# Kernel optimization log

Measured on AMD Instinct MI355X. Metric: run time of the kernel, lower is better.

Reference implementation:

```python
import jax, jax.numpy as jnp
import numpy as np

B, C, H = 256, 5, 13
N_AGENTS = 8192
N_EDGES = 262144
ACT = 21


def setup_inputs() -> dict:
    key = jax.random.key(0)
    ks = jax.random.split(key, 20)
    inp = {
        "x": jax.random.normal(ks[0], (B, C, H, H), jnp.float32),
        "x_msg": jax.random.normal(ks[1], (N_AGENTS,), jnp.float32),
        "edge_index": jax.random.randint(ks[2], (N_EDGES, 2), 0, N_AGENTS, jnp.int64 if jax.config.jax_enable_x64 else jnp.int32),
        "action": jax.random.randint(ks[3], (B,), 0, ACT, jnp.int32),
        # params (orthogonal init approximated by scaled normal; math identical)
        "conv1_w": jax.random.normal(ks[4], (32, 5, 3, 3), jnp.float32) * 0.1,
        "conv1_b": jnp.zeros((32,), jnp.float32),
        "conv2_w": jax.random.normal(ks[5], (64, 32, 3, 3), jnp.float32) * 0.05,
        "conv2_b": jnp.zeros((64,), jnp.float32),
        "fc_w": jax.random.normal(ks[6], (512, 1024), jnp.float32) * 0.03,
        "fc_b": jnp.zeros((512,), jnp.float32),
        "fc_mu_w": jax.random.normal(ks[7], (ACT, 512), jnp.float32) * 0.01,
        "fc_mu_b": jnp.zeros((ACT,), jnp.float32),
        "msg_w": jax.random.normal(ks[8], (N_AGENTS, 512), jnp.float32) * 0.01,
        "msg_b": jnp.zeros((N_AGENTS,), jnp.float32),
        "gcn1_w": jax.random.normal(ks[9], (2, 16), jnp.float32) * 0.5,
        "gcn1_b": jnp.zeros((16,), jnp.float32),
        "gcn2_w": jax.random.normal(ks[10], (16, N_AGENTS), jnp.float32) * 0.1,
        "gcn2_b": jnp.zeros((N_AGENTS,), jnp.float32),
    }
    return inp


def _gcn_norm(edge_index, n):
    # add self-loops; edge_index is (E,2) [src, dst]
    loops = jnp.arange(n, dtype=edge_index.dtype)
    src = jnp.concatenate([edge_index[:, 0], loops])
    dst = jnp.concatenate([edge_index[:, 1], loops])
    deg = jax.ops.segment_sum(jnp.ones_like(src, jnp.float32), dst, num_segments=n)
    dinv = jnp.where(deg > 0, jax.lax.rsqrt(deg), 0.0)
    norm = dinv[src] * dinv[dst]  # [E+n]
    return src, dst, norm


def _gcn_conv(h, src, dst, norm, W, b, n):
    hw = h @ W  # [n, out]
    out = jax.ops.segment_sum(norm[:, None] * hw[src], dst, num_segments=n)
    return out + b


def reference(x, x_msg, edge_index, action, conv1_w, conv1_b, conv2_w, conv2_b,
              fc_w, fc_b, fc_mu_w, fc_mu_b, msg_w, msg_b,
              gcn1_w, gcn1_b, gcn2_w, gcn2_b):
    dn = ("NCHW", "OIHW", "NCHW")
    h = jax.lax.conv_general_dilated(x, conv1_w, (2, 2), "VALID", dimension_numbers=dn)
    h = jax.nn.relu(h + conv1_b[None, :, None, None])  # [B,32,6,6]
    h = jax.lax.conv_general_dilated(h, conv2_w, (1, 1), "VALID", dimension_numbers=dn)
    h = jax.nn.relu(h + conv2_b[None, :, None, None])  # [B,64,4,4]
    h = h.reshape(h.shape[0], -1)  # [B,1024], torch NCHW flatten order
    hidden = jax.nn.relu(h @ fc_w.T + fc_b)  # [B,512]

    logits = hidden @ fc_mu_w.T + fc_mu_b            # [B,21]
    actor_encoding = hidden @ msg_w.T + msg_b        # [B,N]

    # Categorical log_prob / entropy for the given action
    logp = jax.nn.log_softmax(logits, axis=-1)
    log_prob = jnp.take_along_axis(logp, action[:, None], axis=1)[:, 0]
    entropy = -jnp.sum(jnp.exp(logp) * logp, axis=-1)

    # GNN message branch (eval mode: dropout is identity)
    feats = jnp.stack([x_msg, actor_encoding[0]], axis=0).T  # [N,2]
    n = feats.shape[0]
    src, dst, norm = _gcn_norm(edge_index, n)
    g = jax.nn.relu(_gcn_conv(feats, src, dst, norm, gcn1_w, gcn1_b, n))  # [N,16]
    g = _gcn_conv(g, src, dst, norm, gcn2_w, gcn2_b, n)                    # [N,N]
    msg_out = jax.nn.log_softmax(g, axis=1).mean(axis=1)                   # [N]

    return (action, msg_out, log_prob, entropy)
```

## Files before the change

kernel.cpp:

```cpp
#include <hip/hip_runtime.h>
#include <hip/hip_bf16.h>

#define NB 256
#define NACT 21
#define NA 8192
#define NE 262144
#define CSR_CAP 128
#define LOG2E 1.44269504f

#if __has_builtin(__builtin_amdgcn_exp2f)
#define EXP2F(x) __builtin_amdgcn_exp2f(x)
#else
#define EXP2F(x) exp2f(x)
#endif

typedef __attribute__((ext_vector_type(8))) short short8;
typedef __attribute__((ext_vector_type(4))) float float4v;

__device__ inline float wsum64(float v) {
#pragma unroll
  for (int m = 32; m > 0; m >>= 1) v += __shfl_xor(v, m, 64);
  return v;
}

__device__ inline unsigned short f2bf(float f) {
  union { __hip_bfloat16 h; unsigned short u; } cv;
  cv.h = __float2bfloat16(f);
  return cv.u;
}

__global__ __launch_bounds__(512, 2) void k_ic(
    const float* __restrict__ x, const float* __restrict__ c1w, const float* __restrict__ c1b_,
    const float* __restrict__ c2w, unsigned short* c1b, unsigned short* w2abf, int* cnt) {
  __shared__ float sm[3437];
  int t = threadIdx.x, b = blockIdx.x;
  if (b >= 272) {
    int i = (b - 272) * 512 + t;
    w2abf[i] = f2bf(c2w[i]);
    return;
  }
  if (b >= 256) {
    cnt[(b - 256) * 512 + t] = 0;
    return;
  }
  float* xs = sm;
  float* w1s = sm + 845;
  float* c1s = sm + 2285;
  for (int i = t; i < 845; i += 512) xs[i] = x[b * 845 + i];
  for (int i = t; i < 1440; i += 512) w1s[i] = c1w[i];
  __syncthreads();
  for (int idx = t; idx < 1152; idx += 512) {
    int oc = idx / 36, p = idx - oc * 36;
    int oy = p / 6, ox = p - oy * 6;
    float acc = c1b_[oc];
    const float* wp = &w1s[oc * 45];
#pragma unroll
    for (int ic = 0; ic < 5; ic++)
#pragma unroll
      for (int ky = 0; ky < 3; ky++)
#pragma unroll
        for (int kx = 0; kx < 3; kx++)
          acc += xs[ic * 169 + (oy * 2 + ky) * 13 + ox * 2 + kx] * wp[ic * 9 + ky * 3 + kx];
    c1s[idx] = fmaxf(acc, 0.0f);
  }
  __syncthreads();
  for (int i = t; i < 4608; i += 512) {
    int p = i / 288, k = i - p * 288;
    int ic = k / 9, r = k - ic * 9;
    int ky = r / 3, kx = r - ky * 3;
    int oy = p >> 2, ox = p & 3;
    c1b[b * 4608 + i] = f2bf(c1s[ic * 36 + (oy + ky) * 6 + ox + kx]);
  }
}

__global__ __launch_bounds__(512, 2) void k_pc(
    const int* __restrict__ edges, const float* __restrict__ fcw,
    const float* __restrict__ g2w, const float* __restrict__ g2b,
    unsigned short* fcwbf, unsigned short* w2t, float* wpart, int* cnt, int* csr,
    const unsigned short* __restrict__ c1b, const unsigned short* __restrict__ w2abf,
    const float* __restrict__ c2b, unsigned short* h1024bf) {
  __shared__ float sm[288];
  int t = threadIdx.x;
  int wave = t >> 6, lane = t & 63;
  if (blockIdx.x < 512) {
    float (*red)[17] = (float(*)[17])sm;
    float* b2s = sm + 272;
    int blk = blockIdx.x;
    {
      int e = blk * 512 + t;
      int s = edges[2 * e], d = edges[2 * e + 1];
      int slot = atomicAdd(&cnt[d], 1);
      if (slot < CSR_CAP) csr[d * CSR_CAP + slot] = s;
    }
    {
      int base = (blk * 512 + t) * 2;
      float2 v = *(const float2*)&fcw[base];
      fcwbf[base + 0] = f2bf(v.x);
      fcwbf[base + 1] = f2bf(v.y);
    }
    {
      if (t < 256) {
        int jj = t >> 4, k = t & 15;
        int j = blk * 16 + jj;
        float w = g2w[k * 8192 + j];
        w2t[j * 16 + k] = f2bf(w);
        red[jj][k] = w;
      }
      if (t < 16) b2s[t] = g2b[blk * 16 + t];
      __syncthreads();
      if (t < 16) {
        float s = 0.0f;
#pragma unroll
        for (int q = 0; q < 16; q++) s += red[q][t];
        wpart[blk * 17 + t] = s;
      } else if (t == 16) {
        float s = 0.0f;
#pragma unroll
        for (int q = 0; q < 16; q++) s += b2s[q];
        wpart[blk * 17 + 16] = s;
      }
    }
  } else {
    int nb = blockIdx.x - 512;
    int nbase = nb * 256 + wave * 32;
    int m = lane & 15, quad = lane >> 4;
    float4v z = {0.0f, 0.0f, 0.0f, 0.0f};
    float4v acc00 = z, acc01 = z, acc02 = z, acc03 = z;
    float4v acc10 = z, acc11 = z, acc12 = z, acc13 = z;
#pragma unroll
    for (int ks = 0; ks < 9; ks++) {
      int ko = ks * 32 + quad * 8;
      short8 a0 = *(const short8*)&w2abf[(0 * 16 + m) * 288 + ko];
      short8 a1 = *(const short8*)&w2abf[(1 * 16 + m) * 288 + ko];
      short8 a2 = *(const short8*)&w2abf[(2 * 16 + m) * 288 + ko];
      short8 a3 = *(const short8*)&w2abf[(3 * 16 + m) * 288 + ko];
      short8 b0 = *(const short8*)&c1b[(nbase + m) * 288 + ko];
      short8 b1 = *(const short8*)&c1b[(nbase + 16 + m) * 288 + ko];
      acc00 = __builtin_amdgcn_mfma_f32_16x16x32_bf16(a0, b0, acc00, 0, 0, 0);
      acc01 = __builtin_amdgcn_mfma_f32_16x16x32_bf16(a1, b0, acc01, 0, 0, 0);
      acc02 = __builtin_amdgcn_mfma_f32_16x16x32_bf16(a2, b0, acc02, 0, 0, 0);
      acc03 = __builtin_amdgcn_mfma_f32_16x16x32_bf16(a3, b0, acc03, 0, 0, 0);
      acc10 = __builtin_amdgcn_mfma_f32_16x16x32_bf16(a0, b1, acc10, 0, 0, 0);
      acc11 = __builtin_amdgcn_mfma_f32_16x16x32_bf16(a1, b1, acc11, 0, 0, 0);
      acc12 = __builtin_amdgcn_mfma_f32_16x16x32_bf16(a2, b1, acc12, 0, 0, 0);
      acc13 = __builtin_amdgcn_mfma_f32_16x16x32_bf16(a3, b1, acc13, 0, 0, 0);
    }
    float4v accs[2][4] = {{acc00, acc01, acc02, acc03}, {acc10, acc11, acc12, acc13}};
#pragma unroll
    for (int nt = 0; nt < 2; nt++) {
#pragma unroll
      for (int mt = 0; mt < 4; mt++) {
#pragma unroll
        for (int r = 0; r < 4; r++) {
          int oc = mt * 16 + quad * 4 + r;
          int n = nbase + nt * 16 + m;
          int img = n >> 4, pos = n & 15;
          h1024bf[img * 1024 + oc * 16 + pos] =
              f2bf(fmaxf(accs[nt][mt][r] + c2b[oc], 0.0f));
        }
      }
    }
  }
}

__global__ __launch_bounds__(256, 4) void k_fc(
    const int* __restrict__ cnt, const float* __restrict__ x_msg,
    const unsigned short* __restrict__ h1024bf, const unsigned short* __restrict__ fcwbf,
    const float* __restrict__ fcb, const float* __restrict__ wpart,
    float* hidden, float* dinv, float* xs2, float* wsf) {
  __shared__ float red[4][256];
  int t = threadIdx.x, blk = blockIdx.x;
  if (blk == 512) {
    float* part = &red[0][0];
    if (t < 272) {
      int q = t / 17, c = t - q * 17;
      float s = 0.0f;
      for (int r = q; r < 512; r += 16) s += wpart[r * 17 + c];
      part[t] = s;
    }
    __syncthreads();
    if (t < 17) {
      float s = 0.0f;
#pragma unroll
      for (int q = 0; q < 16; q++) s += part[q * 17 + t];
      wsf[t] = s;
    }
    return;
  }
  int wave = t >> 6, lane = t & 63;
  if (blk < 32) {
    int i = blk * 256 + t;
    float d = rsqrtf((float)cnt[i] + 1.0f);
    dinv[i] = d;
    xs2[i] = d * x_msg[i];
  }
  int tr = blk >> 5, tc = blk & 31;
  int m = lane & 15, quad = lane >> 4;
  const unsigned short* ap = &h1024bf[(tr * 16 + m) * 1024 + wave * 256 + quad * 8];
  const unsigned short* bp = &fcwbf[(tc * 16 + m) * 1024 + wave * 256 + quad * 8];
  float4v acc = {0.0f, 0.0f, 0.0f, 0.0f};
#pragma unroll
  for (int i = 0; i < 8; i++) {
    short8 a = *(const short8*)(ap + i * 32);
    short8 b = *(const short8*)(bp + i * 32);
    acc = __builtin_amdgcn_mfma_f32_16x16x32_bf16(a, b, acc, 0, 0, 0);
  }
#pragma unroll
  for (int r = 0; r < 4; r++) red[wave][(quad * 4 + r) * 16 + m] = acc[r];
  __syncthreads();
  {
    float s = red[0][t] + red[1][t] + red[2][t] + red[3][t];
    int gr = tr * 16 + (t >> 4);
    int gc = tc * 16 + (t & 15);
    hidden[gr * 512 + gc] = fmaxf(s + fcb[gc], 0.0f);
  }
}

__global__ __launch_bounds__(512, 2) void k_he(
    const float* __restrict__ hidden, const float* __restrict__ muw,
    const float* __restrict__ mub, const float* __restrict__ msgw,
    const float* __restrict__ msgb, const float* __restrict__ dinv,
    const int* __restrict__ action, float* es2, float* out) {
  __shared__ float muT[10752];
  __shared__ float hrows[2048];
  int t = threadIdx.x, blk = blockIdx.x;
  int wave = t >> 6, lane = t & 63;
  if (blk < 64) {
    int b0 = blk * 4;
    for (int i = t; i < 10752; i += 512) {
      int a = i >> 9, k = i & 511;
      muT[k * 21 + a] = muw[i];
    }
    for (int i = t; i < 2048; i += 512) hrows[i] = hidden[b0 * 512 + i];
    __syncthreads();
    if (wave < 4) {
      int b = b0 + wave;
      float logit = -1e30f;
      if (lane < NACT) {
        float acc = mub[lane];
        const float* hr = &hrows[wave * 512];
        for (int k = 0; k < 512; k++) acc += hr[k] * muT[k * 21 + lane];
        logit = acc;
      }
      float m = logit;
#pragma unroll
      for (int s = 32; s > 0; s >>= 1) m = fmaxf(m, __shfl_xor(m, s, 64));
      float e = (lane < NACT) ? __expf(logit - m) : 0.0f;
      float se = wsum64(e);
      float swl = wsum64(e * logit);
      float lse = m + __logf(se);
      int act = action[b];
      if (lane == 0) {
        out[b] = (float)act;
        out[8704 + b] = lse - swl / se;
      }
      if (lane == act) out[8448 + b] = logit - lse;
    }
  } else {
    int wg = (blk - 64) * 8 + wave;
    for (int j = wg; j < NA; j += 3584) {
      const float* wp = &msgw[j * 512 + lane * 8];
      float4 w0 = *(const float4*)(wp);
      float4 w1 = *(const float4*)(wp + 4);
      float4 h0 = *(const float4*)&hidden[lane * 8];
      float4 h1 = *(const float4*)&hidden[lane * 8 + 4];
      float s = w0.x * h0.x + w0.y * h0.y + w0.z * h0.z + w0.w * h0.w +
                w1.x * h1.x + w1.y * h1.y + w1.z * h1.z + w1.w * h1.w;
      s = wsum64(s);
      if (lane == 0) es2[j] = dinv[j] * (s + msgb[j]);
    }
  }
}

__global__ __launch_bounds__(512, 4) void k_g1(
    const int* __restrict__ cnt, const int* __restrict__ csr,
    const float* __restrict__ dinv, const float* __restrict__ xs2,
    const float* __restrict__ es2, const float* __restrict__ g1w,
    const float* __restrict__ g1b, float* gbuf2) {
  int t = threadIdx.x, blk = blockIdx.x;
  int wave = t >> 6, lane = t & 63;
  int wg = blk * 8 + wave;
#pragma unroll
  for (int rr = 0; rr < 2; rr++) {
    int i = wg * 2 + rr;
    int ci = min(cnt[i], CSR_CAP);
    float di = dinv[i];
    float a0 = 0.0f, a1 = 0.0f;
    for (int e = lane; e < ci; e += 64) {
      int s = csr[i * CSR_CAP + e];
      a0 += xs2[s];
      a1 += es2[s];
    }
    float f0 = (wsum64(a0) + xs2[i]) * di;
    float f1 = (wsum64(a1) + es2[i]) * di;
    if (lane < 16) {
      float gv = fmaxf(f0 * g1w[lane] + f1 * g1w[16 + lane] + g1b[lane], 0.0f);
      gbuf2[i * 16 + lane] = di * gv;
    }
  }
}

__global__ __launch_bounds__(512, 2) void k_msg(
    const int* __restrict__ cnt, const int* __restrict__ csr,
    const float* __restrict__ dinv, const float* __restrict__ gbuf2,
    const float* __restrict__ wsf, const unsigned short* __restrict__ w2t,
    const float* __restrict__ g2b, float* out) {
  __shared__ __align__(16) unsigned short vbf[256];
  __shared__ float vf[256];
  __shared__ float pl[2048];
  __shared__ float sl[128];
  __shared__ float wsfs[17];
  int t = threadIdx.x, blk = blockIdx.x;
  int wave = t >> 6, lane = t & 63;
  int rowbase = blk * 16;
  if (t < 17) wsfs[t] = wsf[t];
  {
    int eq = lane >> 4, c = lane & 15;
#pragma unroll
    for (int rr = 0; rr < 2; rr++) {
      int il = wave * 2 + rr;
      int i = rowbase + il;
      int ci = min(cnt[i], CSR_CAP);
      float di = dinv[i];
      float acc = (eq == 0) ? gbuf2[i * 16 + c] : 0.0f;
      for (int e = eq; e < ci; e += 4) {
        int s = csr[i * CSR_CAP + e];
        acc += gbuf2[s * 16 + c];
      }
      acc *= di;
      acc += __shfl_xor(acc, 16, 64);
      acc += __shfl_xor(acc, 32, 64);
      if (eq == 0) {
        vf[il * 16 + c] = acc;
        vbf[il * 16 + c] = f2bf(acc * LOG2E);
      }
    }
  }
  __syncthreads();
  float myMean = 0.0f;
  if (t < 16) {
    float dot = 0.0f;
#pragma unroll
    for (int c = 0; c < 16; c++) dot += vf[t * 16 + c] * wsfs[c];
    myMean = (dot + wsfs[16]) * (1.0f / 8192.0f);
  }
  {
    int quad = lane >> 4, n = lane & 15;
    int k8 = quad * 8;
    short8 za = {0, 0, 0, 0, 0, 0, 0, 0};
    short8 a1 = za;
    if (quad < 2) a1 = *(const short8*)&vbf[n * 16 + k8];
    float sacc[4];
#pragma unroll
    for (int q = 0; q < 4; q++) sacc[q] = 0.0f;
    int colb = wave * 1024 + n;
    for (int tp = 0; tp < 64; tp += 2) {
      int col1 = colb + tp * 16;
      int col2 = col1 + 16;
      short8 b1 = za, b2 = za;
      if (quad < 2) {
        b1 = *(const short8*)&w2t[col1 * 16 + k8];
        b2 = *(const short8*)&w2t[col2 * 16 + k8];
      }
      float bb1 = g2b[col1] * LOG2E, bb2 = g2b[col2] * LOG2E;
      float4v c1 = {bb1, bb1, bb1, bb1};
      float4v c2 = {bb2, bb2, bb2, bb2};
      float4v s11 = __builtin_amdgcn_mfma_f32_16x16x32_bf16(a1, b1, c1, 0, 0, 0);
      float4v s12 = __builtin_amdgcn_mfma_f32_16x16x32_bf16(a1, b2, c2, 0, 0, 0);
#pragma unroll
      for (int r = 0; r < 4; r++) sacc[r] += EXP2F(s11[r]) + EXP2F(s12[r]);
    }
#pragma unroll
    for (int q = 0; q < 4; q++) {
      int rl = quad * 4 + q;
      pl[rl * 128 + wave * 16 + n] = sacc[q];
    }
  }
  __syncthreads();
  if (t < 128) {
    int r = t >> 3, seg = t & 7;
    int base = r * 128 + seg * 16;
    float ll = 0.0f;
#pragma unroll
    for (int i = 0; i < 16; i++) ll += pl[base + i];
    sl[r * 8 + seg] = ll;
  }
  __syncthreads();
  if (t < 16) {
    float ll = 0.0f;
#pragma unroll
    for (int i = 0; i < 8; i++) ll += sl[t * 8 + i];
    out[256 + rowbase + t] = myMean - __logf(ll);
  }
}

extern "C" void kernel_launch(void* const* d_in, const int* in_sizes, int n_in,
                              void* d_out, int out_size, void* d_ws, size_t ws_size,
                              hipStream_t stream) {
  const float* x     = (const float*)d_in[0];
  const float* x_msg = (const float*)d_in[1];
  const int*   edges = (const int*)d_in[2];
  const int*   action= (const int*)d_in[3];
  const float* c1w   = (const float*)d_in[4];
  const float* c1bb  = (const float*)d_in[5];
  const float* c2w   = (const float*)d_in[6];
  const float* c2b   = (const float*)d_in[7];
  const float* fcw   = (const float*)d_in[8];
  const float* fcb   = (const float*)d_in[9];
  const float* muw   = (const float*)d_in[10];
  const float* mub   = (const float*)d_in[11];
  const float* msgw  = (const float*)d_in[12];
  const float* msgb  = (const float*)d_in[13];
  const float* g1w   = (const float*)d_in[14];
  const float* g1b   = (const float*)d_in[15];
  const float* g2w   = (const float*)d_in[16];
  const float* g2b   = (const float*)d_in[17];
  float* out = (float*)d_out;

  float* ws     = (float*)d_ws;
  unsigned short* h1024bf = (unsigned short*)ws;
  unsigned short* fcwbf   = (unsigned short*)(ws + 131072);
  float* hidden = ws + 393216;
  float* es2    = ws + 524288;
  float* dinv   = ws + 532480;
  float* xs2    = ws + 540672;
  float* gbuf2  = ws + 548864;
  float* wpart  = ws + 679936;
  unsigned short* w2t = (unsigned short*)(ws + 688640);
  int*   cnt    = (int*)(ws + 754176);
  int*   csr    = (int*)(ws + 762368);
  float* wsf    = ws + 1810944;
  unsigned short* c1b   = (unsigned short*)(ws + 1810964);
  unsigned short* w2abf = (unsigned short*)(ws + 2400788);

  k_ic <<<308, 512, 0, stream>>>(x, c1w, c1bb, c2w, c1b, w2abf, cnt);
  k_pc <<<528, 512, 0, stream>>>(edges, fcw, g2w, g2b, fcwbf, w2t, wpart, cnt, csr,
                                 c1b, w2abf, c2b, h1024bf);
  k_fc <<<513, 256, 0, stream>>>(cnt, x_msg, h1024bf, fcwbf, fcb, wpart, hidden, dinv, xs2, wsf);
  k_he <<<512, 512, 0, stream>>>(hidden, muw, mub, msgw, msgb, dinv, action, es2, out);
  k_g1 <<<512, 512, 0, stream>>>(cnt, csr, dinv, xs2, es2, g1w, g1b, gbuf2);
  k_msg<<<512, 512, 0, stream>>>(cnt, csr, dinv, gbuf2, wsf, w2t, g2b, out);
}
```

Measured before the change: 174.2 us.

## Fuse FC layer with actor head and message encoding into one kernel

Merges the FC GEMM kernel and the head/encoding kernel into a single launch. Each block recomputes its 16-row hidden tile in LDS as bf16, so the hidden matrix never goes through global memory. The actor logits move to MFMA, and the message-encoding blocks recompute hidden row 0 redundantly. This drops one launch and the global round-trip but adds redundant FC work across 80 blocks, uses a small grid of 97 blocks, and lowers hidden and mu-weight precision to bf16.

New measurement: 220.6 us. 26.7% more time.

```diff
diff --git a/kernel.cpp b/kernel.cpp
--- a/kernel.cpp
+++ b/kernel.cpp
@@ -27,6 +27,12 @@
   union { __hip_bfloat16 h; unsigned short u; } cv;
   cv.h = __float2bfloat16(f);
   return cv.u;
+}
+
+__device__ inline float bf2f(unsigned short u) {
+  union { unsigned int u; float f; } cv;
+  cv.u = ((unsigned int)u) << 16;
+  return cv.f;
 }
 
 __global__ __launch_bounds__(512, 2) void k_ic(
@@ -163,111 +169,116 @@
   }
 }
 
-__global__ __launch_bounds__(256, 4) void k_fc(
+__global__ __launch_bounds__(512, 2) void k_fhe(
     const int* __restrict__ cnt, const float* __restrict__ x_msg,
     const unsigned short* __restrict__ h1024bf, const unsigned short* __restrict__ fcwbf,
-    const float* __restrict__ fcb, const float* __restrict__ wpart,
-    float* hidden, float* dinv, float* xs2, float* wsf) {
-  __shared__ float red[4][256];
-  int t = threadIdx.x, blk = blockIdx.x;
-  if (blk == 512) {
-    float* part = &red[0][0];
+    const float* __restrict__ fcb, const float* __restrict__ muw, const float* __restrict__ mub,
+    const float* __restrict__ msgw, const float* __restrict__ msgb,
+    const int* __restrict__ action, const float* __restrict__ wpart,
+    float* es2, float* dinv, float* xs2, float* wsf, float* out) {
+  __shared__ __align__(16) unsigned short hidbf[8192];
+  __shared__ float smf[512];
+  int t = threadIdx.x, b = blockIdx.x;
+  int wave = t >> 6, lane = t & 63;
+  if (b >= 96) {
     if (t < 272) {
       int q = t / 17, c = t - q * 17;
       float s = 0.0f;
       for (int r = q; r < 512; r += 16) s += wpart[r * 17 + c];
-      part[t] = s;
+      smf[t] = s;
     }
     __syncthreads();
     if (t < 17) {
       float s = 0.0f;
 #pragma unroll
-      for (int q = 0; q < 16; q++) s += part[q * 17 + t];
+      for (int q = 0; q < 16; q++) s += smf[q * 17 + t];
       wsf[t] = s;
     }
     return;
   }
-  int wave = t >> 6, lane = t & 63;
-  if (blk < 32) {
-    int i = blk * 256 + t;
+  if (b >= 80) {
+    int i = (b - 80) * 512 + t;
     float d = rsqrtf((float)cnt[i] + 1.0f);
     dinv[i] = d;
     xs2[i] = d * x_msg[i];
-  }
-  int tr = blk >> 5, tc = blk & 31;
+    return;
+  }
+  int r0 = (b < 16) ? b * 16 : 0;
   int m = lane & 15, quad = lane >> 4;
-  const unsigned short* ap = &h1024bf[(tr * 16 + m) * 1024 + wave * 256 + quad * 8];
-  const unsigned short* bp = &fcwbf[(tc * 16 + m) * 1024 + wave * 256 + quad * 8];
-  float4v acc = {0.0f, 0.0f, 0.0f, 0.0f};
-#pragma unroll
-  for (int i = 0; i < 8; i++) {
-    short8 a = *(const short8*)(ap + i * 32);
-    short8 b = *(const short8*)(bp + i * 32);
-    acc = __builtin_amdgcn_mfma_f32_16x16x32_bf16(a, b, acc, 0, 0, 0);
-  }
-#pragma unroll
-  for (int r = 0; r < 4; r++) red[wave][(quad * 4 + r) * 16 + m] = acc[r];
-  __syncthreads();
   {
-    float s = red[0][t] + red[1][t] + red[2][t] + red[3][t];
-    int gr = tr * 16 + (t >> 4);
-    int gc = tc * 16 + (t & 15);
-    hidden[gr * 512 + gc] = fmaxf(s + fcb[gc], 0.0f);
-  }
-}
-
-__global__ __launch_bounds__(512, 2) void k_he(
-    const float* __restrict__ hidden, const float* __restrict__ muw,
-    const float* __restrict__ mub, const float* __restrict__ msgw,
-    const float* __restrict__ msgb, const float* __restrict__ dinv,
-    const int* __restrict__ action, float* es2, float* out) {
-  __shared__ float muT[10752];
-  __shared__ float hrows[2048];
-  int t = threadIdx.x, blk = blockIdx.x;
-  int wave = t >> 6, lane = t & 63;
-  if (blk < 64) {
-    int b0 = blk * 4;
-    for (int i = t; i < 10752; i += 512) {
-      int a = i >> 9, k = i & 511;
-      muT[k * 21 + a] = muw[i];
-    }
-    for (int i = t; i < 2048; i += 512) hrows[i] = hidden[b0 * 512 + i];
+    const unsigned short* ap = &h1024bf[(r0 + m) * 1024 + quad * 8];
+#pragma unroll
+    for (int tc = 0; tc < 4; tc++) {
+      int col0 = wave * 64 + tc * 16;
+      const unsigned short* bp = &fcwbf[(col0 + m) * 1024 + quad * 8];
+      float4v acc = {0.0f, 0.0f, 0.0f, 0.0f};
+#pragma unroll
+      for (int ks = 0; ks < 32; ks++) {
+        short8 av = *(const short8*)(ap + ks * 32);
+        short8 bv = *(const short8*)(bp + ks * 32);
+        acc = __builtin_amdgcn_mfma_f32_16x16x32_bf16(av, bv, acc, 0, 0, 0);
+      }
+#pragma unroll
+      for (int r = 0; r < 4; r++) {
+        int i = quad * 4 + r;
+        hidbf[i * 512 + col0 + m] = f2bf(fmaxf(acc[r] + fcb[col0 + m], 0.0f));
+      }
+    }
+  }
+  __syncthreads();
+  if (b < 16) {
+    if (wave < 2) {
+      int col0 = wave * 16;
+      int act_i = col0 + m;
+      float bias = (act_i < NACT) ? mub[act_i] : 0.0f;
+      float4v acc = {bias, bias, bias, bias};
+#pragma unroll
+      for (int ks = 0; ks < 16; ks++) {
+        short8 av = *(const short8*)&hidbf[m * 512 + ks * 32 + quad * 8];
+        short8 bv = {0, 0, 0, 0, 0, 0, 0, 0};
+        if (act_i < NACT) {
+          const float* wp = &muw[act_i * 512 + ks * 32 + quad * 8];
+#pragma unroll
+          for (int q2 = 0; q2 < 8; q2++) bv[q2] = (short)f2bf(wp[q2]);
+        }
+        acc = __builtin_amdgcn_mfma_f32_16x16x32_bf16(av, bv, acc, 0, 0, 0);
+      }
+#pragma unroll
+      for (int r = 0; r < 4; r++) smf[(quad * 4 + r) * 32 + col0 + m] = acc[r];
+    }
     __syncthreads();
-    if (wave < 4) {
-      int b = b0 + wave;
-      float logit = -1e30f;
-      if (lane < NACT) {
-        float acc = mub[lane];
-        const float* hr = &hrows[wave * 512];
-        for (int k = 0; k < 512; k++) acc += hr[k] * muT[k * 21 + lane];
-        logit = acc;
-      }
-      float m = logit;
-#pragma unroll
-      for (int s = 32; s > 0; s >>= 1) m = fmaxf(m, __shfl_xor(m, s, 64));
-      float e = (lane < NACT) ? __expf(logit - m) : 0.0f;
+#pragma unroll
+    for (int rr = 0; rr < 2; rr++) {
+      int rloc = wave * 2 + rr;
+      int bb = r0 + rloc;
+      float logit = (lane < NACT) ? smf[rloc * 32 + lane] : -1e30f;
+      float mx = logit;
+#pragma unroll
+      for (int s = 32; s > 0; s >>= 1) mx = fmaxf(mx, __shfl_xor(mx, s, 64));
+      float e = (lane < NACT) ? __expf(logit - mx) : 0.0f;
       float se = wsum64(e);
       float swl = wsum64(e * logit);
-      float lse = m + __logf(se);
-      int act = action[b];
+      float lse = mx + __logf(se);
+      int act = action[bb];
       if (lane == 0) {
-        out[b] = (float)act;
-        out[8704 + b] = lse - swl / se;
-      }
-      if (lane == act) out[8448 + b] = logit - lse;
+        out[bb] = (float)act;
+        out[8704 + bb] = lse - swl / se;
+      }
+      if (lane == act) out[8448 + bb] = logit - lse;
     }
   } else {
-    int wg = (blk - 64) * 8 + wave;
-    for (int j = wg; j < NA; j += 3584) {
+    float h0[8];
+#pragma unroll
+    for (int q2 = 0; q2 < 8; q2++) h0[q2] = bf2f(hidbf[lane * 8 + q2]);
+    int jbase = (b - 16) * 128 + wave * 16;
+    for (int j = jbase; j < jbase + 16; j++) {
       const float* wp = &msgw[j * 512 + lane * 8];
       float4 w0 = *(const float4*)(wp);
       float4 w1 = *(const float4*)(wp + 4);
-      float4 h0 = *(const float4*)&hidden[lane * 8];
-      float4 h1 = *(const float4*)&hidden[lane * 8 + 4];
-      float s = w0.x * h0.x + w0.y * h0.y + w0.z * h0.z + w0.w * h0.w +
-                w1.x * h1.x + w1.y * h1.y + w1.z * h1.z + w1.w * h1.w;
+      float s = w0.x * h0[0] + w0.y * h0[1] + w0.z * h0[2] + w0.w * h0[3] +
+                w1.x * h0[4] + w1.y * h0[5] + w1.z * h0[6] + w1.w * h0[7];
       s = wsum64(s);
-      if (lane == 0) es2[j] = dinv[j] * (s + msgb[j]);
+      if (lane == 0) es2[j] = rsqrtf((float)cnt[j] + 1.0f) * (s + msgb[j]);
     }
   }
 }
@@ -420,7 +431,6 @@
   float* ws     = (float*)d_ws;
   unsigned short* h1024bf = (unsigned short*)ws;
   unsigned short* fcwbf   = (unsigned short*)(ws + 131072);
-  float* hidden = ws + 393216;
   float* es2    = ws + 524288;
   float* dinv   = ws + 532480;
   float* xs2    = ws + 540672;
@@ -436,8 +446,8 @@
   k_ic <<<308, 512, 0, stream>>>(x, c1w, c1bb, c2w, c1b, w2abf, cnt);
   k_pc <<<528, 512, 0, stream>>>(edges, fcw, g2w, g2b, fcwbf, w2t, wpart, cnt, csr,
                                  c1b, w2abf, c2b, h1024bf);
-  k_fc <<<513, 256, 0, stream>>>(cnt, x_msg, h1024bf, fcwbf, fcb, wpart, hidden, dinv, xs2, wsf);
-  k_he <<<512, 512, 0, stream>>>(hidden, muw, mub, msgw, msgb, dinv, action, es2, out);
+  k_fhe<<<97, 512, 0, stream>>>(cnt, x_msg, h1024bf, fcwbf, fcb, muw, mub, msgw, msgb,
+                                action, wpart, es2, dinv, xs2, wsf, out);
   k_g1 <<<512, 512, 0, stream>>>(cnt, csr, dinv, xs2, es2, g1w, g1b, gbuf2);
   k_msg<<<512, 512, 0, stream>>>(cnt, csr, dinv, gbuf2, wsf, w2t, g2b, out);
 }
```

## Fuse conv2 into FC GEMM via LDS and merge prep kernels

Applied to the files above, without the earlier changes.

Moves the weight-conversion and wpart work into the first kernel, and fuses the conv2 MFMA with the FC GEMM. Each FC block now recomputes its 16-image conv2 tile into shared memory, so the h1024 global round trip is gone. Edge CSR building moves to the fused kernel, and the dinv/xs2 computation moves to k_he, which recomputes rsqrt inline. This removes one kernel launch and a global intermediate. In exchange, the conv2 tile is computed redundantly 32 times, once per column block.

Result: no change. 175.9 us (+1.0%).

```diff
diff --git a/kernel.cpp b/kernel.cpp
--- a/kernel.cpp
+++ b/kernel.cpp
@@ -29,69 +29,18 @@
   return cv.u;
 }
 
-__global__ __launch_bounds__(512, 2) void k_ic(
+__global__ __launch_bounds__(512, 2) void k_ip(
     const float* __restrict__ x, const float* __restrict__ c1w, const float* __restrict__ c1b_,
-    const float* __restrict__ c2w, unsigned short* c1b, unsigned short* w2abf, int* cnt) {
+    const float* __restrict__ c2w, const float* __restrict__ fcw,
+    const float* __restrict__ g2w, const float* __restrict__ g2b,
+    unsigned short* c1b, unsigned short* w2abf, int* cnt,
+    unsigned short* fcwbf, unsigned short* w2t, float* wpart) {
   __shared__ float sm[3437];
   int t = threadIdx.x, b = blockIdx.x;
-  if (b >= 272) {
-    int i = (b - 272) * 512 + t;
-    w2abf[i] = f2bf(c2w[i]);
-    return;
-  }
-  if (b >= 256) {
-    cnt[(b - 256) * 512 + t] = 0;
-    return;
-  }
-  float* xs = sm;
-  float* w1s = sm + 845;
-  float* c1s = sm + 2285;
-  for (int i = t; i < 845; i += 512) xs[i] = x[b * 845 + i];
-  for (int i = t; i < 1440; i += 512) w1s[i] = c1w[i];
-  __syncthreads();
-  for (int idx = t; idx < 1152; idx += 512) {
-    int oc = idx / 36, p = idx - oc * 36;
-    int oy = p / 6, ox = p - oy * 6;
-    float acc = c1b_[oc];
-    const float* wp = &w1s[oc * 45];
-#pragma unroll
-    for (int ic = 0; ic < 5; ic++)
-#pragma unroll
-      for (int ky = 0; ky < 3; ky++)
-#pragma unroll
-        for (int kx = 0; kx < 3; kx++)
-          acc += xs[ic * 169 + (oy * 2 + ky) * 13 + ox * 2 + kx] * wp[ic * 9 + ky * 3 + kx];
-    c1s[idx] = fmaxf(acc, 0.0f);
-  }
-  __syncthreads();
-  for (int i = t; i < 4608; i += 512) {
-    int p = i / 288, k = i - p * 288;
-    int ic = k / 9, r = k - ic * 9;
-    int ky = r / 3, kx = r - ky * 3;
-    int oy = p >> 2, ox = p & 3;
-    c1b[b * 4608 + i] = f2bf(c1s[ic * 36 + (oy + ky) * 6 + ox + kx]);
-  }
-}
-
-__global__ __launch_bounds__(512, 2) void k_pc(
-    const int* __restrict__ edges, const float* __restrict__ fcw,
-    const float* __restrict__ g2w, const float* __restrict__ g2b,
-    unsigned short* fcwbf, unsigned short* w2t, float* wpart, int* cnt, int* csr,
-    const unsigned short* __restrict__ c1b, const unsigned short* __restrict__ w2abf,
-    const float* __restrict__ c2b, unsigned short* h1024bf) {
-  __shared__ float sm[288];
-  int t = threadIdx.x;
-  int wave = t >> 6, lane = t & 63;
-  if (blockIdx.x < 512) {
+  if (b >= 308) {
     float (*red)[17] = (float(*)[17])sm;
     float* b2s = sm + 272;
-    int blk = blockIdx.x;
-    {
-      int e = blk * 512 + t;
-      int s = edges[2 * e], d = edges[2 * e + 1];
-      int slot = atomicAdd(&cnt[d], 1);
-      if (slot < CSR_CAP) csr[d * CSR_CAP + slot] = s;
-    }
+    int blk = b - 308;
     {
       int base = (blk * 512 + t) * 2;
       float2 v = *(const float2*)&fcw[base];
@@ -120,10 +69,85 @@
         wpart[blk * 17 + 16] = s;
       }
     }
-  } else {
-    int nb = blockIdx.x - 512;
-    int nbase = nb * 256 + wave * 32;
-    int m = lane & 15, quad = lane >> 4;
+    return;
+  }
+  if (b >= 272) {
+    int i = (b - 272) * 512 + t;
+    w2abf[i] = f2bf(c2w[i]);
+    return;
+  }
+  if (b >= 256) {
+    cnt[(b - 256) * 512 + t] = 0;
+    return;
+  }
+  float* xs = sm;
+  float* w1s = sm + 845;
+  float* c1s = sm + 2285;
+  for (int i = t; i < 845; i += 512) xs[i] = x[b * 845 + i];
+  for (int i = t; i < 1440; i += 512) w1s[i] = c1w[i];
+  __syncthreads();
+  for (int idx = t; idx < 1152; idx += 512) {
+    int oc = idx / 36, p = idx - oc * 36;
+    int oy = p / 6, ox = p - oy * 6;
+    float acc = c1b_[oc];
+    const float* wp = &w1s[oc * 45];
+#pragma unroll
+    for (int ic = 0; ic < 5; ic++)
+#pragma unroll
+      for (int ky = 0; ky < 3; ky++)
+#pragma unroll
+        for (int kx = 0; kx < 3; kx++)
+          acc += xs[ic * 169 + (oy * 2 + ky) * 13 + ox * 2 + kx] * wp[ic * 9 + ky * 3 + kx];
+    c1s[idx] = fmaxf(acc, 0.0f);
+  }
+  __syncthreads();
+  for (int i = t; i < 4608; i += 512) {
+    int p = i / 288, k = i - p * 288;
+    int ic = k / 9, r = k - ic * 9;
+    int ky = r / 3, kx = r - ky * 3;
+    int oy = p >> 2, ox = p & 3;
+    c1b[b * 4608 + i] = f2bf(c1s[ic * 36 + (oy + ky) * 6 + ox + kx]);
+  }
+}
+
+__global__ __launch_bounds__(512, 2) void k_cf(
+    const int* __restrict__ edges, int* cnt, int* csr,
+    const unsigned short* __restrict__ c1b, const unsigned short* __restrict__ w2abf,
+    const float* __restrict__ c2b, const unsigned short* __restrict__ fcwbf,
+    const float* __restrict__ fcb, const float* __restrict__ wpart,
+    float* hidden, float* wsf) {
+  __shared__ __align__(16) unsigned short hs[16384];
+  __shared__ float red[2048];
+  int t = threadIdx.x, blk = blockIdx.x;
+  int wave = t >> 6, lane = t & 63;
+  int m = lane & 15, quad = lane >> 4;
+  if (blk >= 1024) {
+    if (t < 272) {
+      int q = t / 17, c = t - q * 17;
+      float s = 0.0f;
+      for (int r = q; r < 512; r += 16) s += wpart[r * 17 + c];
+      red[t] = s;
+    }
+    __syncthreads();
+    if (t < 17) {
+      float s = 0.0f;
+#pragma unroll
+      for (int q = 0; q < 16; q++) s += red[q * 17 + t];
+      wsf[t] = s;
+    }
+    return;
+  }
+  if (blk >= 512) {
+    int e = (blk - 512) * 512 + t;
+    int s = edges[2 * e], d = edges[2 * e + 1];
+    int slot = atomicAdd(&cnt[d], 1);
+    if (slot < CSR_CAP) csr[d * CSR_CAP + slot] = s;
+    return;
+  }
+  int tr = blk >> 5, tc = blk & 31;
+  {
+    int nlb = wave * 32;
+    int nbase = tr * 256 + nlb;
     float4v z = {0.0f, 0.0f, 0.0f, 0.0f};
     float4v acc00 = z, acc01 = z, acc02 = z, acc03 = z;
     float4v acc10 = z, acc11 = z, acc12 = z, acc13 = z;
@@ -153,78 +177,55 @@
 #pragma unroll
         for (int r = 0; r < 4; r++) {
           int oc = mt * 16 + quad * 4 + r;
-          int n = nbase + nt * 16 + m;
-          int img = n >> 4, pos = n & 15;
-          h1024bf[img * 1024 + oc * 16 + pos] =
+          int nl = nlb + nt * 16 + m;
+          hs[(nl >> 4) * 1024 + oc * 16 + (nl & 15)] =
               f2bf(fmaxf(accs[nt][mt][r] + c2b[oc], 0.0f));
         }
       }
     }
   }
-}
-
-__global__ __launch_bounds__(256, 4) void k_fc(
-    const int* __restrict__ cnt, const float* __restrict__ x_msg,
-    const unsigned short* __restrict__ h1024bf, const unsigned short* __restrict__ fcwbf,
-    const float* __restrict__ fcb, const float* __restrict__ wpart,
-    float* hidden, float* dinv, float* xs2, float* wsf) {
-  __shared__ float red[4][256];
-  int t = threadIdx.x, blk = blockIdx.x;
-  if (blk == 512) {
-    float* part = &red[0][0];
-    if (t < 272) {
-      int q = t / 17, c = t - q * 17;
+  __syncthreads();
+  {
+    const unsigned short* ap = &hs[m * 1024 + wave * 128 + quad * 8];
+    const unsigned short* bp = &fcwbf[(tc * 16 + m) * 1024 + wave * 128 + quad * 8];
+    float4v acc = {0.0f, 0.0f, 0.0f, 0.0f};
+#pragma unroll
+    for (int ks = 0; ks < 4; ks++) {
+      short8 av = *(const short8*)(ap + ks * 32);
+      short8 bv = *(const short8*)(bp + ks * 32);
+      acc = __builtin_amdgcn_mfma_f32_16x16x32_bf16(av, bv, acc, 0, 0, 0);
+    }
+#pragma unroll
+    for (int r = 0; r < 4; r++) red[wave * 256 + (quad * 4 + r) * 16 + m] = acc[r];
+    __syncthreads();
+    if (t < 256) {
       float s = 0.0f;
-      for (int r = q; r < 512; r += 16) s += wpart[r * 17 + c];
-      part[t] = s;
-    }
-    __syncthreads();
-    if (t < 17) {
-      float s = 0.0f;
-#pragma unroll
-      for (int q = 0; q < 16; q++) s += part[q * 17 + t];
-      wsf[t] = s;
-    }
-    return;
-  }
-  int wave = t >> 6, lane = t & 63;
-  if (blk < 32) {
-    int i = blk * 256 + t;
-    float d = rsqrtf((float)cnt[i] + 1.0f);
-    dinv[i] = d;
-    xs2[i] = d * x_msg[i];
-  }
-  int tr = blk >> 5, tc = blk & 31;
-  int m = lane & 15, quad = lane >> 4;
-  const unsigned short* ap = &h1024bf[(tr * 16 + m) * 1024 + wave * 256 + quad * 8];
-  const unsigned short* bp = &fcwbf[(tc * 16 + m) * 1024 + wave * 256 + quad * 8];
-  float4v acc = {0.0f, 0.0f, 0.0f, 0.0f};
-#pragma unroll
-  for (int i = 0; i < 8; i++) {
-    short8 a = *(const short8*)(ap + i * 32);
-    short8 b = *(const short8*)(bp + i * 32);
-    acc = __builtin_amdgcn_mfma_f32_16x16x32_bf16(a, b, acc, 0, 0, 0);
-  }
-#pragma unroll
-  for (int r = 0; r < 4; r++) red[wave][(quad * 4 + r) * 16 + m] = acc[r];
-  __syncthreads();
-  {
-    float s = red[0][t] + red[1][t] + red[2][t] + red[3][t];
-    int gr = tr * 16 + (t >> 4);
-    int gc = tc * 16 + (t & 15);
-    hidden[gr * 512 + gc] = fmaxf(s + fcb[gc], 0.0f);
+#pragma unroll
+      for (int w = 0; w < 8; w++) s += red[w * 256 + t];
+      int gr = tr * 16 + (t >> 4);
+      int gc = tc * 16 + (t & 15);
+      hidden[gr * 512 + gc] = fmaxf(s + fcb[gc], 0.0f);
+    }
   }
 }
 
 __global__ __launch_bounds__(512, 2) void k_he(
     const float* __restrict__ hidden, const float* __restrict__ muw,
     const float* __restrict__ mub, const float* __restrict__ msgw,
-    const float* __restrict__ msgb, const float* __restrict__ dinv,
-    const int* __restrict__ action, float* es2, float* out) {
+    const float* __restrict__ msgb, const int* __restrict__ cnt,
+    const float* __restrict__ x_msg, const int* __restrict__ action,
+    float* es2, float* dinv, float* xs2, float* out) {
   __shared__ float muT[10752];
   __shared__ float hrows[2048];
   int t = threadIdx.x, blk = blockIdx.x;
   int wave = t >> 6, lane = t & 63;
+  if (blk >= 512) {
+    int i = (blk - 512) * 512 + t;
+    float d = rsqrtf((float)cnt[i] + 1.0f);
+    dinv[i] = d;
+    xs2[i] = d * x_msg[i];
+    return;
+  }
   if (blk < 64) {
     int b0 = blk * 4;
     for (int i = t; i < 10752; i += 512) {
@@ -242,13 +243,13 @@
         for (int k = 0; k < 512; k++) acc += hr[k] * muT[k * 21 + lane];
         logit = acc;
       }
-      float m = logit;
-#pragma unroll
-      for (int s = 32; s > 0; s >>= 1) m = fmaxf(m, __shfl_xor(m, s, 64));
-      float e = (lane < NACT) ? __expf(logit - m) : 0.0f;
+      float mx = logit;
+#pragma unroll
+      for (int s = 32; s > 0; s >>= 1) mx = fmaxf(mx, __shfl_xor(mx, s, 64));
+      float e = (lane < NACT) ? __expf(logit - mx) : 0.0f;
       float se = wsum64(e);
       float swl = wsum64(e * logit);
-      float lse = m + __logf(se);
+      float lse = mx + __logf(se);
       int act = action[b];
       if (lane == 0) {
         out[b] = (float)act;
@@ -267,7 +268,7 @@
       float s = w0.x * h0.x + w0.y * h0.y + w0.z * h0.z + w0.w * h0.w +
                 w1.x * h1.x + w1.y * h1.y + w1.z * h1.z + w1.w * h1.w;
       s = wsum64(s);
-      if (lane == 0) es2[j] = dinv[j] * (s + msgb[j]);
+      if (lane == 0) es2[j] = rsqrtf((float)cnt[j] + 1.0f) * (s + msgb[j]);
     }
   }
 }
@@ -418,7 +419,6 @@
   float* out = (float*)d_out;
 
   float* ws     = (float*)d_ws;
-  unsigned short* h1024bf = (unsigned short*)ws;
   unsigned short* fcwbf   = (unsigned short*)(ws + 131072);
   float* hidden = ws + 393216;
   float* es2    = ws + 524288;
@@ -433,11 +433,12 @@
   unsigned short* c1b   = (unsigned short*)(ws + 1810964);
   unsigned short* w2abf = (unsigned short*)(ws + 2400788);
 
-  k_ic <<<308, 512, 0, stream>>>(x, c1w, c1bb, c2w, c1b, w2abf, cnt);
-  k_pc <<<528, 512, 0, stream>>>(edges, fcw, g2w, g2b, fcwbf, w2t, wpart, cnt, csr,
-                                 c1b, w2abf, c2b, h1024bf);
-  k_fc <<<513, 256, 0, stream>>>(cnt, x_msg, h1024bf, fcwbf, fcb, wpart, hidden, dinv, xs2, wsf);
-  k_he <<<512, 512, 0, stream>>>(hidden, muw, mub, msgw, msgb, dinv, action, es2, out);
+  k_ip <<<820, 512, 0, stream>>>(x, c1w, c1bb, c2w, fcw, g2w, g2b,
+                                 c1b, w2abf, cnt, fcwbf, w2t, wpart);
+  k_cf <<<1025, 512, 0, stream>>>(edges, cnt, csr, c1b, w2abf, c2b,
+                                  fcwbf, fcb, wpart, hidden, wsf);
+  k_he <<<528, 512, 0, stream>>>(hidden, muw, mub, msgw, msgb, cnt, x_msg,
+                                 action, es2, dinv, xs2, out);
   k_g1 <<<512, 512, 0, stream>>>(cnt, csr, dinv, xs2, es2, g1w, g1b, gbuf2);
   k_msg<<<512, 512, 0, stream>>>(cnt, csr, dinv, gbuf2, wsf, w2t, g2b, out);
 }
```
